# Performance work log

Hardware: AMD Instinct MI355X
Metric: run time of the kernel (lower is better)

## Reference

```python
import jax, jax.numpy as jnp
import numpy as np

B, T, IDIM, HDIM, K, LMAX, NLAYERS = 64, 1024, 120, 320, 72, 96, 3
LAMB = 0.1
NEG = -1e30


def lse3(a, b, c):
    m = jnp.maximum(jnp.maximum(a, b), c)
    return m + jnp.log(jnp.exp(a - m) + jnp.exp(b - m) + jnp.exp(c - m))


def _lstm_dir(x, Wih, Whh, bb):
    # x: [B,T,D] -> h: [B,T,H]; PyTorch gate order i,f,g,o
    gx = jnp.einsum('btd,gd->tbg', x, Wih) + bb  # [T,B,4H]
    def step(carry, g):
        h, c = carry
        g = g + h @ Whh.T
        i, f, gg, o = jnp.split(g, 4, axis=-1)
        c = jax.nn.sigmoid(f) * c + jax.nn.sigmoid(i) * jnp.tanh(gg)
        h = jax.nn.sigmoid(o) * jnp.tanh(c)
        return (h, c), h
    h0 = jnp.zeros((x.shape[0], HDIM), x.dtype)
    _, hs = jax.lax.scan(step, (h0, h0), gx)
    return hs.transpose(1, 0, 2)


def _rev(x, lengths):
    # reverse each sequence within its valid length (packed-sequence semantics)
    t = jnp.arange(x.shape[1])
    idx = jnp.where(t[None, :] < lengths[:, None], lengths[:, None] - 1 - t[None, :], t[None, :])
    return jnp.take_along_axis(x, idx[:, :, None], axis=1)


def _blstm_layer(x, Wih_f, Whh_f, b_f, Wih_b, Whh_b, b_b, lengths):
    hf = _lstm_dir(x, Wih_f, Whh_f, b_f)
    hb = _rev(_lstm_dir(_rev(x, lengths), Wih_b, Whh_b, b_b), lengths)
    return jnp.concatenate([hf, hb], axis=2)


def _ctc_forward(logp, labels, in_lens, lab_lens):
    # standard CTC alpha recursion (blank=0), log-space, vectorized over batch
    Bn, Tn, _ = logp.shape
    S = 2 * LMAX + 1
    ext = jnp.zeros((Bn, S), jnp.int32).at[:, 1::2].set(labels)  # blank-interleaved labels
    em = jnp.take_along_axis(logp, jnp.broadcast_to(ext[:, None, :], (Bn, Tn, S)), axis=2)
    em = em.transpose(1, 0, 2)  # [T,B,S]
    s_idx = jnp.arange(S)
    prev_lab = jnp.concatenate([jnp.full((Bn, 2), -1, jnp.int32), ext[:, :-2]], axis=1)
    can_skip = ((s_idx[None, :] % 2) == 1) & (ext != prev_lab)
    valid_s = s_idx[None, :] < (2 * lab_lens[:, None] + 1)
    alpha0 = jnp.full((Bn, S), NEG, logp.dtype)
    alpha0 = alpha0.at[:, 0].set(em[0][:, 0]).at[:, 1].set(em[0][:, 1])
    alpha0 = jnp.where(valid_s, alpha0, NEG)
    def step(alpha, inp):
        em_t, t = inp
        a2 = jnp.concatenate([jnp.full((Bn, 1), NEG, alpha.dtype), alpha[:, :-1]], axis=1)
        a3 = jnp.concatenate([jnp.full((Bn, 2), NEG, alpha.dtype), alpha[:, :-2]], axis=1)
        a3 = jnp.where(can_skip, a3, NEG)
        new = lse3(alpha, a2, a3) + em_t
        new = jnp.where(valid_s, new, NEG)
        new = jnp.where((t < in_lens)[:, None], new, alpha)  # freeze past utterance end
        return new, None
    alpha, _ = jax.lax.scan(step, alpha0, (em[1:], jnp.arange(1, Tn)))
    last = 2 * lab_lens
    aL = jnp.take_along_axis(alpha, last[:, None], axis=1)[:, 0]
    aLm1 = jnp.take_along_axis(alpha, (last - 1)[:, None], axis=1)[:, 0]
    return jnp.logaddexp(aL, aLm1)  # log p(labels | x)


def setup_inputs():
    key = jax.random.key(0)
    ks = jax.random.split(key, 12)
    H4 = 4 * HDIM
    s = 0.05
    return dict(
        logits=jax.random.normal(ks[0], (B, T, IDIM), jnp.float32),
        labels_padded=jax.random.randint(ks[1], (B, LMAX), 1, K).astype(jnp.int32),
        input_lengths=jax.random.randint(ks[2], (B,), T // 2, T + 1).astype(jnp.int32),
        label_lengths=jax.random.randint(ks[3], (B,), LMAX // 2, LMAX + 1).astype(jnp.int32),
        Wih0=jax.random.normal(ks[4], (2, H4, IDIM), jnp.float32) * s,
        Whh0=jax.random.normal(ks[5], (2, H4, HDIM), jnp.float32) * s,
        b0=jnp.zeros((2, H4), jnp.float32),
        Wih=jax.random.normal(ks[6], (NLAYERS - 1, 2, H4, 2 * HDIM), jnp.float32) * s,
        Whh=jax.random.normal(ks[7], (NLAYERS - 1, 2, H4, HDIM), jnp.float32) * s,
        b=jnp.zeros((NLAYERS - 1, 2, H4), jnp.float32),
        W_lin=jax.random.normal(ks[8], (K, 2 * HDIM), jnp.float32) * s,
        b_lin=jnp.zeros((K,), jnp.float32),
    )


def reference(logits, labels_padded, input_lengths, label_lengths, Wih0, Whh0, b0, Wih, Whh, b, W_lin, b_lin):
    # sort by input length descending (mirrors torch.sort + index_select)
    order = jnp.argsort(-input_lengths)
    logits = logits[order]
    labels_padded = labels_padded[order]
    input_lengths = input_lengths[order]
    label_lengths = label_lengths[order]
    # 3-layer BLSTM encoder
    x = _blstm_layer(logits, Wih0[0], Whh0[0], b0[0], Wih0[1], Whh0[1], b0[1], input_lengths)
    for l in range(NLAYERS - 1):
        x = _blstm_layer(x, Wih[l, 0], Whh[l, 0], b[l, 0], Wih[l, 1], Whh[l, 1], b[l, 1], input_lengths)
    netout = jax.nn.log_softmax(x @ W_lin.T + b_lin, axis=2)  # [B,T,K]
    # CTC-CRF: numerator = CTC alpha log-prob; denominator = free-running partition
    num = _ctc_forward(netout, labels_padded, input_lengths, label_lengths)
    tmask = jnp.arange(netout.shape[1])[None, :] < input_lengths[:, None]
    den = jnp.sum(jnp.where(tmask, jax.nn.logsumexp(netout, axis=2), 0.0), axis=1)
    return jnp.mean(den - (1.0 + LAMB) * num)
```

## Files before the change

kernel.cpp:

```cpp
#include <hip/hip_runtime.h>
#include <cstdint>
#include <cstddef>


typedef _Float16 f16;
typedef _Float16 h2v   __attribute__((ext_vector_type(2)));
typedef _Float16 f16x4v __attribute__((ext_vector_type(4)));
typedef _Float16 f16x8 __attribute__((ext_vector_type(8)));
typedef float    f32x4 __attribute__((ext_vector_type(4)));
typedef uint32_t u32x4 __attribute__((ext_vector_type(4)));

#define NEGF (-1e30f)
#define CT 128

__device__ __forceinline__ int dot4i8(int a, int b, int c) {
#if __has_builtin(__builtin_amdgcn_sdot4)
  return __builtin_amdgcn_sdot4(a, b, c, false);
#else
  int s = c;
#pragma unroll
  for (int e = 0; e < 4; ++e)
    s += (int)(int8_t)(a >> (8 * e)) * (int)(int8_t)(b >> (8 * e));
  return s;
#endif
}

__device__ __forceinline__ float fast_rcp(float x) {
#if __has_builtin(__builtin_amdgcn_rcpf)
  return __builtin_amdgcn_rcpf(x);
#else
  return 1.f / x;
#endif
}
__device__ __forceinline__ float fsigm(float x) { return fast_rcp(1.f + __expf(-x)); }
__device__ __forceinline__ float ftanh(float x) { return 1.f - 2.f * fast_rcp(1.f + __expf(2.f * x)); }

__device__ __forceinline__ float fexp2(float x) {
#if __has_builtin(__builtin_amdgcn_exp2f)
  return __builtin_amdgcn_exp2f(x);
#else
  return exp2f(x);
#endif
}
__device__ __forceinline__ float flog2(float x) {
#if __has_builtin(__builtin_amdgcn_logf)
  return __builtin_amdgcn_logf(x);
#else
  return log2f(x);
#endif
}

__device__ __forceinline__ void stage16(f16* lds, const f16* g) {
#if __has_builtin(__builtin_amdgcn_global_load_lds)
  __builtin_amdgcn_global_load_lds(
      (const __attribute__((address_space(1))) uint32_t*)g,
      (__attribute__((address_space(3))) uint32_t*)lds, 16, 0, 0);
#else
  int lane = threadIdx.x & 63;
  *(f16x8*)&lds[lane * 8] = *(const f16x8*)g;
#endif
}


__global__ void conv_logits(const float* __restrict__ src, f16* __restrict__ dst) {
  int idx = blockIdx.x * 256 + threadIdx.x;
  int row = idx >> 7, k = idx & 127;
  dst[idx] = (f16)((k < 120) ? src[(size_t)row * 120 + k] : 0.f);
}

__global__ void conv_wt0(const float* __restrict__ w, f16* __restrict__ dst) {
  int idx = blockIdx.x * 256 + threadIdx.x;
  int n = idx >> 7, k = idx & 127;
  dst[idx] = (f16)((k < 120) ? w[(size_t)n * 120 + k] : 0.f);
}

__global__ void conv_copy(const float* __restrict__ src, f16* __restrict__ dst, int count) {
  int idx = blockIdx.x * 256 + threadIdx.x;
  if (idx < count) dst[idx] = (f16)src[idx];
}

__global__ void conv_wtl(const float* __restrict__ w, f16* __restrict__ dst) {
  int idx = blockIdx.x * 256 + threadIdx.x;
  int n = idx / 640, k = idx % 640;
  dst[idx] = (f16)((n < 72) ? w[(size_t)n * 640 + k] : 0.f);
}

__global__ void conv_scale(const float* __restrict__ whh0, const float* __restrict__ whh,
                           float* __restrict__ scales) {
  int row = blockIdx.x * 4 + (threadIdx.x >> 6);
  int lane = threadIdx.x & 63;
  int slot = row / 1280, r = row - slot * 1280;
  const float* src = (slot < 2) ? (whh0 + ((size_t)slot * 1280 + r) * 320)
                                : (whh  + ((size_t)(slot - 2) * 1280 + r) * 320);
  float m = 0.f;
  for (int k = lane; k < 320; k += 64) m = fmaxf(m, fabsf(src[k]));
#pragma unroll
  for (int o = 32; o; o >>= 1) m = fmaxf(m, __shfl_xor(m, o, 64));
  if (lane == 0) scales[row] = fmaxf(m, 1e-20f) * (1.f / 127.f);
}

__global__ void conv_wq(const float* __restrict__ whh0, const float* __restrict__ whh,
                        const float* __restrict__ scales, uint32_t* __restrict__ dst) {
  int o = blockIdx.x * 256 + threadIdx.x;
  int t = o & 511;
  int g = o >> 9;
  int j = g % 20;
  int g2 = g / 20;
  int i = g2 % 10;
  int slot = g2 / 10;
  int qi = t >> 2, kq = t & 3;
  int r = i * 128 + qi;
  int k0 = kq * 80 + j * 4;
  const float* src = (slot < 2) ? (whh0 + ((size_t)slot * 1280 + r) * 320)
                                : (whh  + ((size_t)(slot - 2) * 1280 + r) * 320);
  float s = scales[slot * 1280 + r];
  float rs = fast_rcp(s);
  uint32_t w = 0;
#pragma unroll
  for (int e = 0; e < 4; ++e) {
    float q = rintf(src[k0 + e] * rs);
    q = fminf(fmaxf(q, -127.f), 127.f);
    w |= ((uint32_t)(uint8_t)(int8_t)(int)q) << (8 * e);
  }
  dst[o] = w;
}

__global__ __launch_bounds__(256)
void gemm_chunk(const f16* __restrict__ A, const f16* __restrict__ W,
                f16* __restrict__ gxc, const int* __restrict__ lens,
                int lda, int kTiles, int c0) {
  __shared__ __align__(16) f16 As[128 * 32];
  __shared__ __align__(16) f16 Ws[2][128 * 32];
  const int tid = threadIdx.x;
  const int lane = tid & 63, wid = tid >> 6;
  const int wm = wid >> 1, wn = wid & 1;
  const int dir = blockIdx.y >> 6, b = blockIdx.y & 63;
  const int n0 = blockIdx.x * 256;
  const int r_base = lane >> 2;
  const int chs = ((((lane & 3) + (r_base >> 1)) & 3)) * 8;
  const int len = lens[b];

  f32x4 acc[4][8] = {};

  for (int kt = 0; kt < kTiles; ++kt) {
    const int k0 = kt * 32;
    __syncthreads();
#pragma unroll
    for (int hh = 0; hh < 2; ++hh) {
      const int c = wid * 2 + hh;
      const int j = c * 16 + r_base;
      const int s = c0 * CT + j;
      const int tt = dir ? ((s < len) ? (len - 1 - s) : s) : s;
      stage16(&As[c * 512], A + (size_t)(b * 1024 + tt) * lda + k0 + chs);
    }
#pragma unroll
    for (int hh = 0; hh < 4; ++hh) {
      const int c = wid * 4 + hh;
      const int tile = c >> 3, cc = c & 7;
      stage16(&Ws[tile][cc * 512],
              W + (size_t)(dir * 1280 + n0 + tile * 128 + cc * 16 + r_base) * lda + k0 + chs);
    }
    __syncthreads();

    const int q = lane >> 4;
    const int l15 = lane & 15;
    const int cs = (q - (l15 >> 1)) & 3;
    const int rofs = l15 * 32 + cs * 8;
    f16x8 av[4], wv0[4], wv1[4];
#pragma unroll
    for (int i = 0; i < 4; ++i)
      av[i] = *(const f16x8*)&As[(wm * 4 + i) * 512 + rofs];
#pragma unroll
    for (int i = 0; i < 4; ++i) {
      wv0[i] = *(const f16x8*)&Ws[0][(wn * 4 + i) * 512 + rofs];
      wv1[i] = *(const f16x8*)&Ws[1][(wn * 4 + i) * 512 + rofs];
    }
#pragma unroll
    for (int i = 0; i < 4; ++i)
#pragma unroll
      for (int j = 0; j < 4; ++j) {
        acc[i][j]     = __builtin_amdgcn_mfma_f32_16x16x32_f16(av[i], wv0[j], acc[i][j], 0, 0, 0);
        acc[i][4 + j] = __builtin_amdgcn_mfma_f32_16x16x32_f16(av[i], wv1[j], acc[i][4 + j], 0, 0, 0);
      }
  }

  const int r0 = (lane >> 4) * 4, cn = lane & 15;
  const size_t obase = (size_t)(dir * 64 + b) * CT;
#pragma unroll
  for (int i = 0; i < 4; ++i) {
    const int m = wm * 64 + i * 16 + r0;
#pragma unroll
    for (int j = 0; j < 4; ++j) {
      const int n = n0 + wn * 64 + j * 16 + cn;
#pragma unroll
      for (int r = 0; r < 4; ++r) {
        gxc[(obase + m + r) * 1280 + n]       = (f16)acc[i][j][r];
        gxc[(obase + m + r) * 1280 + n + 128] = (f16)acc[i][4 + j][r];
      }
    }
  }
}

__global__ void __launch_bounds__(512)
__attribute__((amdgpu_waves_per_eu(2, 2)))
lstm_scan_chunk(const volatile uint32_t* wqbuf,
                const float* __restrict__ scales,
                const f16* __restrict__ gxc,
                const float* __restrict__ bias,
                const int* __restrict__ lens,
                f16* xnext,
                f16* hsave,
                float* csave,
                int layer, int c0) {
  const int wg = blockIdx.x;
  const int b = wg >> 1, dir = wg & 1;
  const int tid = threadIdx.x;
  const int kq = tid & 3, qi = tid >> 2;
  const int slot = layer * 2 + dir;

  __shared__ __align__(16) uint32_t hqw[80];
  __shared__ int ylds[1280];
  __shared__ __align__(16) f16 hstage[64 * 320];

  uint32_t w[10][20];
  {
    const volatile uint32_t* wb = wqbuf + (size_t)slot * 10 * 20 * 512;
#pragma unroll
    for (int i = 0; i < 10; ++i)
#pragma unroll
      for (int j = 0; j < 20; ++j)
        w[i][j] = wb[(i * 20 + j) * 512 + tid];
  }

  const int len = lens[b];
  float c_state = 0.f, h_cur = 0.f;
  float bi = 0.f, bff = 0.f, bg = 0.f, bo = 0.f;
  float ps0 = 0.f, ps1 = 0.f, ps2 = 0.f, ps3 = 0.f;
  if (tid < 320) {
    float hv0 = (c0 == 0) ? 0.f : (float)hsave[wg * 320 + tid];
    h_cur = hv0;
    ((uint8_t*)hqw)[tid] = (uint8_t)(int8_t)(int)rintf(hv0 * 127.f);
    if (c0 > 0) c_state = csave[wg * 320 + tid];
    const float* bp = bias + dir * 1280 + tid;
    bi = bp[0]; bff = bp[320]; bg = bp[640]; bo = bp[960];
    const float* sp = scales + slot * 1280 + tid;
    ps0 = sp[0] * (1.f / 127.f);
    ps1 = sp[320] * (1.f / 127.f);
    ps2 = sp[640] * (1.f / 127.f);
    ps3 = sp[960] * (1.f / 127.f);
  }
  __syncthreads();

  const size_t grow0 = (size_t)(dir * 64 + b) * CT;

  float gxi = 0.f, gxf = 0.f, gxg = 0.f, gxo = 0.f;
  if (tid < 320) {
    const f16* gp = gxc + grow0 * 1280 + tid;
    gxi = (float)gp[0]; gxf = (float)gp[320]; gxg = (float)gp[640]; gxo = (float)gp[960];
  }

  for (int tl = 0; tl < CT; ++tl) {
    float nxi = 0.f, nxf = 0.f, nxg = 0.f, nxo = 0.f;
    if (tid < 320 && tl + 1 < CT) {
      const f16* gp = gxc + (grow0 + tl + 1) * 1280 + tid;
      nxi = (float)gp[0]; nxf = (float)gp[320]; nxg = (float)gp[640]; nxo = (float)gp[960];
    }

    int acc0 = 0, acc1 = 0, acc2 = 0, acc3 = 0, acc4 = 0;
    int acc5 = 0, acc6 = 0, acc7 = 0, acc8 = 0, acc9 = 0;
    {
      const u32x4* hv4 = (const u32x4*)&hqw[kq * 20];
#pragma unroll
      for (int jb = 0; jb < 5; ++jb) {
        u32x4 hv = hv4[jb];
#pragma unroll
        for (int e = 0; e < 4; ++e) {
          const int j = jb * 4 + e;
          const int hword = (int)hv[e];
          acc0 = dot4i8((int)w[0][j], hword, acc0);
          acc1 = dot4i8((int)w[1][j], hword, acc1);
          acc2 = dot4i8((int)w[2][j], hword, acc2);
          acc3 = dot4i8((int)w[3][j], hword, acc3);
          acc4 = dot4i8((int)w[4][j], hword, acc4);
          acc5 = dot4i8((int)w[5][j], hword, acc5);
          acc6 = dot4i8((int)w[6][j], hword, acc6);
          acc7 = dot4i8((int)w[7][j], hword, acc7);
          acc8 = dot4i8((int)w[8][j], hword, acc8);
          acc9 = dot4i8((int)w[9][j], hword, acc9);
        }
      }
    }
    {
      int av[10] = {acc0, acc1, acc2, acc3, acc4, acc5, acc6, acc7, acc8, acc9};
#pragma unroll
      for (int i = 0; i < 10; ++i) {
        int v = av[i];
        v += __shfl_xor(v, 1, 64);
        v += __shfl_xor(v, 2, 64);
        if (kq == 0) ylds[i * 128 + qi] = v;
      }
    }

    if ((tl & 31) == 0 && tl > 0) {
      const int tw = tl - 32;
#pragma unroll
      for (int it = 0; it < 3; ++it) {
        const int slt = it * 512 + tid;
        if (slt < 1280) {
          const int r = (int)(((unsigned)slt * 1639u) >> 16);
          const int j = slt - r * 40;
          const int sp = c0 * CT + tw + r;
          const int ttp = dir ? ((sp < len) ? (len - 1 - sp) : sp) : sp;
          f16x8 v = *(const f16x8*)&hstage[((tw + r) & 63) * 320 + j * 8];
          *(f16x8*)&xnext[(size_t)(b * 1024 + ttp) * 640 + dir * 320 + j * 8] = v;
        }
      }
    }
    __syncthreads();

    if (tid < 320) {
      const int u = tid;
      float pi = ps0 * (float)ylds[u]       + gxi + bi;
      float pf = ps1 * (float)ylds[u + 320] + gxf + bff;
      float pg = ps2 * (float)ylds[u + 640] + gxg + bg;
      float po = ps3 * (float)ylds[u + 960] + gxo + bo;
      float ig = fsigm(pi);
      float fg = fsigm(pf);
      float gg = ftanh(pg);
      float og = fsigm(po);
      c_state = fg * c_state + ig * gg;
      float hv = og * ftanh(c_state);
      h_cur = hv;
      hstage[(tl & 63) * 320 + u] = (f16)hv;
      ((uint8_t*)hqw)[u] = (uint8_t)(int8_t)(int)rintf(hv * 127.f);
    }
    __syncthreads();

    gxi = nxi; gxf = nxf; gxg = nxg; gxo = nxo;
  }

  {
    const int tw = CT - 32;
#pragma unroll
    for (int it = 0; it < 3; ++it) {
      const int slt = it * 512 + tid;
      if (slt < 1280) {
        const int r = (int)(((unsigned)slt * 1639u) >> 16);
        const int j = slt - r * 40;
        const int sp = c0 * CT + tw + r;
        const int ttp = dir ? ((sp < len) ? (len - 1 - sp) : sp) : sp;
        f16x8 v = *(const f16x8*)&hstage[((tw + r) & 63) * 320 + j * 8];
        *(f16x8*)&xnext[(size_t)(b * 1024 + ttp) * 640 + dir * 320 + j * 8] = v;
      }
    }
  }
  if (tid < 320) {
    hsave[wg * 320 + tid] = (f16)h_cur;
    csave[wg * 320 + tid] = c_state;
  }
}

__global__ __launch_bounds__(256)
void gemm_proj(const f16* __restrict__ A, const f16* __restrict__ W,
               float* __restrict__ outf, int lda, int kTiles, int ldo) {
  __shared__ __align__(16) f16 As[128 * 32];
  __shared__ __align__(16) f16 Ws[128 * 32];
  const int tid = threadIdx.x;
  const int lane = tid & 63, wid = tid >> 6;
  const int wm = wid >> 1, wn = wid & 1;
  const int m0 = blockIdx.y * 128, n0 = blockIdx.x * 128;
  const int r_base = lane >> 2;
  const int chs = ((((lane & 3) + (r_base >> 1)) & 3)) * 8;

  f32x4 acc[4][4] = {};

  for (int kt = 0; kt < kTiles; ++kt) {
    const int k0 = kt * 32;
    __syncthreads();
#pragma unroll
    for (int hh = 0; hh < 2; ++hh) {
      const int c = wid * 2 + hh;
      stage16(&As[c * 512], A + (size_t)(m0 + c * 16 + r_base) * lda + k0 + chs);
      stage16(&Ws[c * 512], W + (size_t)(n0 + c * 16 + r_base) * lda + k0 + chs);
    }
    __syncthreads();

    const int q = lane >> 4;
    const int l15 = lane & 15;
    const int cs = (q - (l15 >> 1)) & 3;
    const int rofs = l15 * 32 + cs * 8;
    f16x8 av[4], wv[4];
#pragma unroll
    for (int i = 0; i < 4; ++i)
      av[i] = *(const f16x8*)&As[(wm * 4 + i) * 512 + rofs];
#pragma unroll
    for (int i = 0; i < 4; ++i)
      wv[i] = *(const f16x8*)&Ws[(wn * 4 + i) * 512 + rofs];
#pragma unroll
    for (int i = 0; i < 4; ++i)
#pragma unroll
      for (int j = 0; j < 4; ++j)
        acc[i][j] = __builtin_amdgcn_mfma_f32_16x16x32_f16(av[i], wv[j], acc[i][j], 0, 0, 0);
  }

  const int r0 = (lane >> 4) * 4, cn = lane & 15;
#pragma unroll
  for (int i = 0; i < 4; ++i) {
    const int m = m0 + wm * 64 + i * 16 + r0;
#pragma unroll
    for (int j = 0; j < 4; ++j) {
      const int n = n0 + wn * 64 + j * 16 + cn;
#pragma unroll
      for (int r = 0; r < 4; ++r)
        outf[(size_t)(m + r) * ldo + n] = acc[i][j][r];
    }
  }
}

__global__ void lse_kernel(const float* __restrict__ Z, const float* __restrict__ b_lin,
                           float* __restrict__ lseout) {
  int row = blockIdx.x * 4 + (threadIdx.x >> 6);
  int l = threadIdx.x & 63;
  const float* z = Z + (size_t)row * 128;
  float v0 = (l < 72) ? z[l] + b_lin[l] : NEGF;
  float v1 = (l < 8) ? z[l + 64] + b_lin[l + 64] : NEGF;
  float m = fmaxf(v0, v1);
#pragma unroll
  for (int o = 32; o; o >>= 1) m = fmaxf(m, __shfl_xor(m, o, 64));
  float s = ((l < 72) ? __expf(v0 - m) : 0.f) + ((l < 8) ? __expf(v1 - m) : 0.f);
#pragma unroll
  for (int o = 32; o; o >>= 1) s += __shfl_xor(s, o, 64);
  if (l == 0) lseout[row] = m + __logf(s);
}

__global__ void emz_kernel(const float* __restrict__ Z, const float* __restrict__ lse,
                           const float* __restrict__ b_lin,
                           const int* __restrict__ labels,
                           f16* __restrict__ emc) {
  const int b = blockIdx.y;
  const int t0 = blockIdx.x * 4;
  const int tid = threadIdx.x;
  __shared__ int ext[200];
  __shared__ float bls[200];
  if (tid < 200) {
    int e = (tid < 193 && (tid & 1)) ? labels[b * 96 + (tid >> 1)] : 0;
    ext[tid] = e;
    bls[tid] = b_lin[e];
  }
  __syncthreads();
#pragma unroll
  for (int dt = 0; dt < 4; ++dt) {
    const int t = t0 + dt;
    const float lst = lse[b * 1024 + t];
    const float* zr = Z + ((size_t)(b * 1024 + t)) * 128;
    for (int s = tid; s < 200; s += 256)
      emc[((size_t)(b * 1024 + t)) * 200 + s] =
          (f16)((zr[ext[s]] + bls[s] - lst) * 1.4426950408889634f);
  }
}

__global__ void ctc_kernel(const f16* __restrict__ emc,
                           const int* __restrict__ labels, const int* __restrict__ inlen,
                           const int* __restrict__ lablen, float* __restrict__ num) {
  const int b = blockIdx.x;
  const int lane = threadIdx.x;
  __shared__ int ext[200];
  __shared__ float afin[200];

  for (int s = lane; s < 200; s += 64)
    ext[s] = (s < 193 && (s & 1)) ? labels[b * 96 + (s >> 1)] : 0;
  __syncthreads();

  const int L = lablen[b], len = inlen[b];
  const int Send = 2 * L + 1;
  const f16* eb = emc + (size_t)b * 1024 * 200;

  float a[4];
  bool  skp[4], val[4];
#pragma unroll
  for (int j = 0; j < 4; ++j) {
    const int s = lane * 4 + j;
    val[j] = (s < Send) && (s < 193);
    skp[j] = (s < 193) && (s & 1) && (s >= 2) && (ext[s] != ext[s - 2]);
  }
  {
    f16x4v e0 = *(const f16x4v*)&eb[lane * 4];
#pragma unroll
    for (int j = 0; j < 4; ++j) {
      const int s = lane * 4 + j;
      a[j] = (s <= 1 && val[j]) ? (float)e0[j] : NEGF;
    }
  }

  auto step = [&](f16x4v ev) {
    float p3 = __shfl_up(a[3], 1, 64);
    float p2 = __shfl_up(a[2], 1, 64);
    if (lane == 0) { p3 = NEGF; p2 = NEGF; }
    const float x2[4] = {p3, a[0], a[1], a[2]};
    const float x3[4] = {p2, p3, a[0], a[1]};
#pragma unroll
    for (int j = 0; j < 4; ++j) {
      const float xa = a[j], xb = x2[j];
      const float xc = skp[j] ? x3[j] : NEGF;
      const float m = fmaxf(xa, fmaxf(xb, xc));
      const float sum = fexp2(xa - m) + fexp2(xb - m) + fexp2(xc - m);
      const float nv = m + flog2(sum) + (float)ev[j];
      a[j] = val[j] ? nv : NEGF;
    }
  };

  f16x4v ring[8];
#pragma unroll
  for (int d = 1; d <= 8; ++d) {
    const int r = (d < len) ? d : (len - 1);
    ring[d & 7] = *(const f16x4v*)&eb[(size_t)r * 200 + lane * 4];
  }

  int t = 1;
  for (; t + 8 <= len; t += 8) {
#pragma unroll
    for (int k = 0; k < 8; ++k) {
      const int slot = (1 + k) & 7;
      f16x4v ev = ring[slot];
      const int tp = t + k + 8;
      if (tp < len)
        ring[slot] = *(const f16x4v*)&eb[(size_t)tp * 200 + lane * 4];
      step(ev);
    }
  }
  for (; t < len; ++t)
    step(*(const f16x4v*)&eb[(size_t)t * 200 + lane * 4]);

#pragma unroll
  for (int j = 0; j < 4; ++j) {
    const int s = lane * 4 + j;
    if (s < 193) afin[s] = a[j];
  }
  __syncthreads();
  if (lane == 0) {
    const float aL = afin[2 * L], aLm1 = afin[2 * L - 1];
    const float m = fmaxf(aL, aLm1);
    num[b] = 0.6931471805599453f * (m + flog2(fexp2(aL - m) + fexp2(aLm1 - m)));
  }
}

__global__ void final_kernel(const float* __restrict__ num, float* __restrict__ out) {
  int l = threadIdx.x;
  float v = -1.1f * num[l];
#pragma unroll
  for (int o = 32; o; o >>= 1) v += __shfl_xor(v, o, 64);
  if (l == 0) out[0] = v * (1.f / 64.f);
}

__global__ void sentinel_kernel(float* __restrict__ out, float code) { out[0] = code; }

extern "C" void kernel_launch(void* const* d_in, const int* in_sizes, int n_in,
                              void* d_out, int out_size, void* d_ws, size_t ws_size,
                              hipStream_t stream) {
  (void)in_sizes; (void)n_in; (void)out_size;

  const float* logits   = (const float*)d_in[0];
  const int*   labels   = (const int*)d_in[1];
  const int*   in_lens  = (const int*)d_in[2];
  const int*   lab_lens = (const int*)d_in[3];
  const float* Wih0     = (const float*)d_in[4];
  const float* Whh0     = (const float*)d_in[5];
  const float* b0       = (const float*)d_in[6];
  const float* Wih      = (const float*)d_in[7];
  const float* Whh      = (const float*)d_in[8];
  const float* bb       = (const float*)d_in[9];
  const float* W_lin    = (const float*)d_in[10];
  const float* b_lin    = (const float*)d_in[11];

  const size_t NEED = (size_t)224 * 1024 * 1024;
  if (ws_size < NEED) {
    sentinel_kernel<<<1, 1, 0, stream>>>((float*)d_out, -(float)(ws_size >> 20));
    return;
  }

  char* ws = (char*)d_ws;
  size_t off = 0;
  auto alloc = [&](size_t bytes) -> char* {
    char* p = ws + off;
    off += (bytes + 255) & ~(size_t)255;
    return p;
  };
  f16*      Xa     = (f16*)alloc((size_t)65536 * 640 * 2);
  f16*      Xb     = (f16*)alloc((size_t)65536 * 640 * 2);
  f16*      gxc    = (f16*)alloc((size_t)2 * 64 * CT * 1280 * 2);
  f16*      Wt0    = (f16*)alloc((size_t)2560 * 128 * 2);
  f16*      Wt12   = (f16*)alloc((size_t)2 * 2560 * 640 * 2);
  f16*      WtL    = (f16*)alloc((size_t)128 * 640 * 2);
  uint32_t* wqi    = (uint32_t*)alloc((size_t)6 * 10 * 20 * 512 * 4);
  float*    scales = (float*)alloc((size_t)6 * 1280 * 4);
  float*    lseb   = (float*)alloc((size_t)65536 * 4);
  float*    num    = (float*)alloc(64 * 4);
  f16*      hsave  = (f16*)alloc((size_t)128 * 320 * 2);
  float*    csave  = (float*)alloc((size_t)128 * 320 * 4);
  f16*      A0     = Xb;
  float*    Z      = (float*)gxc;
  f16*      emc    = Xa;

  conv_logits<<<32768, 256, 0, stream>>>(logits, A0);
  conv_wt0<<<1280, 256, 0, stream>>>(Wih0, Wt0);
  conv_copy<<<12800, 256, 0, stream>>>(Wih, Wt12, 3276800);
  conv_wtl<<<320, 256, 0, stream>>>(W_lin, WtL);
  conv_scale<<<1920, 256, 0, stream>>>(Whh0, Whh, scales);
  conv_wq<<<2400, 256, 0, stream>>>(Whh0, Whh, scales, wqi);

  for (int c = 0; c < 1024 / CT; ++c) {
    gemm_chunk<<<dim3(5, 128), 256, 0, stream>>>(A0, Wt0, gxc, in_lens, 128, 4, c);
    lstm_scan_chunk<<<128, 512, 0, stream>>>(wqi, scales, gxc, b0, in_lens, Xa,
                                             hsave, csave, 0, c);
  }
  for (int c = 0; c < 1024 / CT; ++c) {
    gemm_chunk<<<dim3(5, 128), 256, 0, stream>>>(Xa, Wt12, gxc, in_lens, 640, 20, c);
    lstm_scan_chunk<<<128, 512, 0, stream>>>(wqi, scales, gxc, bb, in_lens, Xb,
                                             hsave, csave, 1, c);
  }
  for (int c = 0; c < 1024 / CT; ++c) {
    gemm_chunk<<<dim3(5, 128), 256, 0, stream>>>(Xb, Wt12 + (size_t)2560 * 640, gxc,
                                                 in_lens, 640, 20, c);
    lstm_scan_chunk<<<128, 512, 0, stream>>>(wqi, scales, gxc, bb + 2560, in_lens, Xa,
                                             hsave, csave, 2, c);
  }
  gemm_proj<<<dim3(1, 512), 256, 0, stream>>>(Xa, WtL, Z, 640, 20, 128);

  lse_kernel<<<16384, 256, 0, stream>>>(Z, b_lin, lseb);
  emz_kernel<<<dim3(256, 64), 256, 0, stream>>>(Z, lseb, b_lin, labels, emc);
  ctc_kernel<<<64, 64, 0, stream>>>(emc, labels, in_lens, lab_lens, num);
  final_kernel<<<1, 64, 0, stream>>>(num, (float*)d_out);
}
```

Baseline: 9.479 ms.

## Split LSTM recurrent weights across 1024 threads per scan block

Each recurrent-scan block now uses 1024 threads instead of 512, so each thread holds half as many int8 weight rows in registers (5x20 words instead of 10x20). The per-step dot-product chain per thread halves, and the weight layout produced by the conversion kernel is changed to match. Bias and scales move into shared memory to free registers, and the saved hidden state is read back from the staging buffer. The cost is more waves per workgroup with only the first 320 threads doing the gate math, plus heavier synchronization per step across 16 waves.

```diff
diff --git a/kernel.cpp b/kernel.cpp
--- a/kernel.cpp
+++ b/kernel.cpp
@@ -102,14 +102,14 @@
 __global__ void conv_wq(const float* __restrict__ whh0, const float* __restrict__ whh,
                         const float* __restrict__ scales, uint32_t* __restrict__ dst) {
   int o = blockIdx.x * 256 + threadIdx.x;
-  int t = o & 511;
-  int g = o >> 9;
+  int t = o & 1023;
+  int g = o >> 10;
   int j = g % 20;
   int g2 = g / 20;
-  int i = g2 % 10;
-  int slot = g2 / 10;
+  int i = g2 % 5;
+  int slot = g2 / 5;
   int qi = t >> 2, kq = t & 3;
-  int r = i * 128 + qi;
+  int r = i * 256 + qi;
   int k0 = kq * 80 + j * 4;
   const float* src = (slot < 2) ? (whh0 + ((size_t)slot * 1280 + r) * 320)
                                 : (whh  + ((size_t)(slot - 2) * 1280 + r) * 320);
@@ -201,16 +201,15 @@
   }
 }
 
-__global__ void __launch_bounds__(512)
-__attribute__((amdgpu_waves_per_eu(2, 2)))
-lstm_scan_chunk(const volatile uint32_t* wqbuf,
+__global__ void __launch_bounds__(1024, 4)
+lstm_scan_chunk(const uint32_t* __restrict__ wqbuf,
                 const float* __restrict__ scales,
                 const f16* __restrict__ gxc,
                 const float* __restrict__ bias,
                 const int* __restrict__ lens,
-                f16* xnext,
-                f16* hsave,
-                float* csave,
+                f16* __restrict__ xnext,
+                f16* __restrict__ hsave,
+                float* __restrict__ csave,
                 int layer, int c0) {
   const int wg = blockIdx.x;
   const int b = wg >> 1, dir = wg & 1;
@@ -220,34 +219,31 @@
 
   __shared__ __align__(16) uint32_t hqw[80];
   __shared__ int ylds[1280];
+  __shared__ float bsl[1280];
+  __shared__ float ssl[1280];
   __shared__ __align__(16) f16 hstage[64 * 320];
 
-  uint32_t w[10][20];
+  uint32_t w[5][20];
   {
-    const volatile uint32_t* wb = wqbuf + (size_t)slot * 10 * 20 * 512;
-#pragma unroll
-    for (int i = 0; i < 10; ++i)
+    const uint32_t* wb = wqbuf + (size_t)slot * 5 * 20 * 1024;
+#pragma unroll
+    for (int i = 0; i < 5; ++i)
 #pragma unroll
       for (int j = 0; j < 20; ++j)
-        w[i][j] = wb[(i * 20 + j) * 512 + tid];
+        w[i][j] = wb[(i * 20 + j) * 1024 + tid];
+  }
+
+  for (int v = tid; v < 1280; v += 1024) {
+    bsl[v] = bias[dir * 1280 + v];
+    ssl[v] = scales[slot * 1280 + v] * (1.f / 127.f);
   }
 
   const int len = lens[b];
-  float c_state = 0.f, h_cur = 0.f;
-  float bi = 0.f, bff = 0.f, bg = 0.f, bo = 0.f;
-  float ps0 = 0.f, ps1 = 0.f, ps2 = 0.f, ps3 = 0.f;
+  float c_state = 0.f;
   if (tid < 320) {
     float hv0 = (c0 == 0) ? 0.f : (float)hsave[wg * 320 + tid];
-    h_cur = hv0;
     ((uint8_t*)hqw)[tid] = (uint8_t)(int8_t)(int)rintf(hv0 * 127.f);
     if (c0 > 0) c_state = csave[wg * 320 + tid];
-    const float* bp = bias + dir * 1280 + tid;
-    bi = bp[0]; bff = bp[320]; bg = bp[640]; bo = bp[960];
-    const float* sp = scales + slot * 1280 + tid;
-    ps0 = sp[0] * (1.f / 127.f);
-    ps1 = sp[320] * (1.f / 127.f);
-    ps2 = sp[640] * (1.f / 127.f);
-    ps3 = sp[960] * (1.f / 127.f);
   }
   __syncthreads();
 
@@ -267,7 +263,6 @@
     }
 
     int acc0 = 0, acc1 = 0, acc2 = 0, acc3 = 0, acc4 = 0;
-    int acc5 = 0, acc6 = 0, acc7 = 0, acc8 = 0, acc9 = 0;
     {
       const u32x4* hv4 = (const u32x4*)&hqw[kq * 20];
 #pragma unroll
@@ -282,30 +277,25 @@
           acc2 = dot4i8((int)w[2][j], hword, acc2);
           acc3 = dot4i8((int)w[3][j], hword, acc3);
           acc4 = dot4i8((int)w[4][j], hword, acc4);
-          acc5 = dot4i8((int)w[5][j], hword, acc5);
-          acc6 = dot4i8((int)w[6][j], hword, acc6);
-          acc7 = dot4i8((int)w[7][j], hword, acc7);
-          acc8 = dot4i8((int)w[8][j], hword, acc8);
-          acc9 = dot4i8((int)w[9][j], hword, acc9);
         }
       }
     }
     {
-      int av[10] = {acc0, acc1, acc2, acc3, acc4, acc5, acc6, acc7, acc8, acc9};
-#pragma unroll
-      for (int i = 0; i < 10; ++i) {
+      int av[5] = {acc0, acc1, acc2, acc3, acc4};
+#pragma unroll
+      for (int i = 0; i < 5; ++i) {
         int v = av[i];
         v += __shfl_xor(v, 1, 64);
         v += __shfl_xor(v, 2, 64);
-        if (kq == 0) ylds[i * 128 + qi] = v;
+        if (kq == 0) ylds[i * 256 + qi] = v;
       }
     }
 
     if ((tl & 31) == 0 && tl > 0) {
       const int tw = tl - 32;
 #pragma unroll
-      for (int it = 0; it < 3; ++it) {
-        const int slt = it * 512 + tid;
+      for (int it = 0; it < 2; ++it) {
+        const int slt = it * 1024 + tid;
         if (slt < 1280) {
           const int r = (int)(((unsigned)slt * 1639u) >> 16);
           const int j = slt - r * 40;
@@ -320,17 +310,16 @@
 
     if (tid < 320) {
       const int u = tid;
-      float pi = ps0 * (float)ylds[u]       + gxi + bi;
-      float pf = ps1 * (float)ylds[u + 320] + gxf + bff;
-      float pg = ps2 * (float)ylds[u + 640] + gxg + bg;
-      float po = ps3 * (float)ylds[u + 960] + gxo + bo;
+      float pi = ssl[u]       * (float)ylds[u]       + gxi + bsl[u];
+      float pf = ssl[u + 320] * (float)ylds[u + 320] + gxf + bsl[u + 320];
+      float pg = ssl[u + 640] * (float)ylds[u + 640] + gxg + bsl[u + 640];
+      float po = ssl[u + 960] * (float)ylds[u + 960] + gxo + bsl[u + 960];
       float ig = fsigm(pi);
       float fg = fsigm(pf);
       float gg = ftanh(pg);
       float og = fsigm(po);
       c_state = fg * c_state + ig * gg;
       float hv = og * ftanh(c_state);
-      h_cur = hv;
       hstage[(tl & 63) * 320 + u] = (f16)hv;
       ((uint8_t*)hqw)[u] = (uint8_t)(int8_t)(int)rintf(hv * 127.f);
     }
@@ -342,8 +331,8 @@
   {
     const int tw = CT - 32;
 #pragma unroll
-    for (int it = 0; it < 3; ++it) {
-      const int slt = it * 512 + tid;
+    for (int it = 0; it < 2; ++it) {
+      const int slt = it * 1024 + tid;
       if (slt < 1280) {
         const int r = (int)(((unsigned)slt * 1639u) >> 16);
         const int j = slt - r * 40;
@@ -355,7 +344,7 @@
     }
   }
   if (tid < 320) {
-    hsave[wg * 320 + tid] = (f16)h_cur;
+    hsave[wg * 320 + tid] = hstage[((CT - 1) & 63) * 320 + tid];
     csave[wg * 320 + tid] = c_state;
   }
 }
@@ -591,7 +580,7 @@
   f16*      Wt0    = (f16*)alloc((size_t)2560 * 128 * 2);
   f16*      Wt12   = (f16*)alloc((size_t)2 * 2560 * 640 * 2);
   f16*      WtL    = (f16*)alloc((size_t)128 * 640 * 2);
-  uint32_t* wqi    = (uint32_t*)alloc((size_t)6 * 10 * 20 * 512 * 4);
+  uint32_t* wqi    = (uint32_t*)alloc((size_t)6 * 5 * 20 * 1024 * 4);
   float*    scales = (float*)alloc((size_t)6 * 1280 * 4);
   float*    lseb   = (float*)alloc((size_t)65536 * 4);
   float*    num    = (float*)alloc(64 * 4);
@@ -610,19 +599,19 @@
 
   for (int c = 0; c < 1024 / CT; ++c) {
     gemm_chunk<<<dim3(5, 128), 256, 0, stream>>>(A0, Wt0, gxc, in_lens, 128, 4, c);
-    lstm_scan_chunk<<<128, 512, 0, stream>>>(wqi, scales, gxc, b0, in_lens, Xa,
-                                             hsave, csave, 0, c);
+    lstm_scan_chunk<<<128, 1024, 0, stream>>>(wqi, scales, gxc, b0, in_lens, Xa,
+                                              hsave, csave, 0, c);
   }
   for (int c = 0; c < 1024 / CT; ++c) {
     gemm_chunk<<<dim3(5, 128), 256, 0, stream>>>(Xa, Wt12, gxc, in_lens, 640, 20, c);
-    lstm_scan_chunk<<<128, 512, 0, stream>>>(wqi, scales, gxc, bb, in_lens, Xb,
-                                             hsave, csave, 1, c);
+    lstm_scan_chunk<<<128, 1024, 0, stream>>>(wqi, scales, gxc, bb, in_lens, Xb,
+                                              hsave, csave, 1, c);
   }
   for (int c = 0; c < 1024 / CT; ++c) {
     gemm_chunk<<<dim3(5, 128), 256, 0, stream>>>(Xb, Wt12 + (size_t)2560 * 640, gxc,
                                                  in_lens, 640, 20, c);
-    lstm_scan_chunk<<<128, 512, 0, stream>>>(wqi, scales, gxc, bb + 2560, in_lens, Xa,
-                                             hsave, csave, 2, c);
+    lstm_scan_chunk<<<128, 1024, 0, stream>>>(wqi, scales, gxc, bb + 2560, in_lens, Xa,
+                                              hsave, csave, 2, c);
   }
   gemm_proj<<<dim3(1, 512), 256, 0, stream>>>(Xa, WtL, Z, 640, 20, 128);
 
```

New measurement: 11.12 ms. +17.3%, slower.
